# Performance work log

Hardware: AMD Instinct MI355X
Metric: run time of the kernel (lower is better)

The kernel has to match this reference:

```python
import jax, jax.numpy as jnp
import numpy as np

GROUPS = 32
EPS = 1e-5


def setup_inputs() -> dict:
    key = jax.random.key(0)
    ks = jax.random.split(key, 3)
    B, C, H, W, D = 2, 512, 32, 32, 32
    x = jax.random.normal(ks[0], (B, C, H, W, D), dtype=jnp.float32)
    # 1x1 Conv3d weights squeezed to 2-D matrices; fan-in scaled init
    qkv_w = jax.random.normal(ks[1], (3 * C, C), dtype=jnp.float32) / np.sqrt(C)
    qkv_b = jnp.zeros((3 * C,), dtype=jnp.float32)
    proj_w = jax.random.normal(ks[2], (C, C), dtype=jnp.float32) / np.sqrt(C)
    proj_b = jnp.zeros((C,), dtype=jnp.float32)
    gn_w = jnp.ones((C,), dtype=jnp.float32)
    gn_b = jnp.zeros((C,), dtype=jnp.float32)
    return {"x": x, "gn_w": gn_w, "gn_b": gn_b, "qkv_w": qkv_w,
            "qkv_b": qkv_b, "proj_w": proj_w, "proj_b": proj_b}


def _group_norm(x, w, b):
    B, C = x.shape[0], x.shape[1]
    xg = x.reshape(B, GROUPS, C // GROUPS, -1)  # [B, G, C/G, N]
    mean = xg.mean(axis=(2, 3), keepdims=True)
    var = xg.var(axis=(2, 3), keepdims=True)
    xn = ((xg - mean) * jax.lax.rsqrt(var + EPS)).reshape(x.shape)
    shape = (1, C) + (1,) * (x.ndim - 2)
    return xn * w.reshape(shape) + b.reshape(shape)


def reference(x, gn_w, gn_b, qkv_w, qkv_b, proj_w, proj_b):
    B, C, H, W, D = x.shape
    N = H * W * D
    xn = _group_norm(x, gn_w, gn_b)
    xf = xn.reshape(B, C, N)
    # 1x1 conv3d == channel-mixing matmul over flattened spatial tokens
    qkv = jnp.einsum('oc,bcn->bon', qkv_w, xf) + qkv_b[None, :, None]
    q, k, v = jnp.split(qkv, 3, axis=1)  # each [B, C, N]
    scale = 1.0 / (C ** 0.5)
    # NOTE: faithful to source -- attention matrix is [B, C, C] (channel attention)
    attn = jax.nn.softmax(jnp.einsum('bcn,bdn->bcd', q, k) * scale, axis=-1)
    out = jnp.einsum('bcd,bdn->bcn', attn, v)  # [B, C, N]
    proj = jnp.einsum('oc,bcn->bon', proj_w, out) + proj_b[None, :, None]
    return x + proj.reshape(B, C, H, W, D)
```

## Files before the change

### kernel.cpp

```cpp
#include <hip/hip_runtime.h>
#include <cstdint>


typedef unsigned short u16;
typedef unsigned int u32;
typedef __bf16 bf16x8 __attribute__((ext_vector_type(8)));
typedef float f4 __attribute__((ext_vector_type(4)));

#define N_SP 32768
#define C_CH 512
#define NB 2
#define KSPLIT 32
#define LSTR 40

__device__ __forceinline__ float b2f(u16 h){
  union { float f; u32 u; } v; v.u = ((u32)h) << 16; return v.f;
}
__device__ __forceinline__ u16 f2b(float f){
  union { float f; u32 u; } v; v.f = f;
  u32 u = v.u;
  return (u16)((u + 0x7fffu + ((u >> 16) & 1u)) >> 16);
}
__device__ __forceinline__ void split(float v, u16& h, u16& l){
  h = f2b(v);
  l = f2b(v - b2f(h));
}

__global__ void k_zero(float* __restrict__ p, long n){
  long i = (long)blockIdx.x*256 + threadIdx.x;
  if(i < n) p[i] = 0.f;
}

__global__ __launch_bounds__(256) void k_stats(const float* __restrict__ x,
                                               float* __restrict__ cs, float* __restrict__ cq){
  const long bc = blockIdx.x;
  const float* p = x + bc * (long)N_SP;
  const int t = threadIdx.x;
  float s = 0.f, q = 0.f;
  for(int i=0;i<32;i++){
    float4 v = *(const float4*)(p + i*1024 + t*4);
    s += v.x + v.y + v.z + v.w;
    q += v.x*v.x + v.y*v.y + v.z*v.z + v.w*v.w;
  }
  for(int off=32; off; off>>=1){ s += __shfl_down(s, off, 64); q += __shfl_down(q, off, 64); }
  __shared__ float rs[4], rq[4];
  int lane = t & 63, wv = t >> 6;
  if(lane==0){ rs[wv]=s; rq[wv]=q; }
  __syncthreads();
  if(t==0){ cs[bc] = rs[0]+rs[1]+rs[2]+rs[3]; cq[bc] = rq[0]+rq[1]+rq[2]+rq[3]; }
}

__global__ void k_gn(const float* __restrict__ cs, const float* __restrict__ cq,
                     const float* __restrict__ gw, const float* __restrict__ gb,
                     float* __restrict__ s_, float* __restrict__ t_, float* __restrict__ rxn){
  int i = blockIdx.x*blockDim.x + threadIdx.x;
  if(i >= NB*C_CH) return;
  int b = i >> 9, c = i & 511, g = c >> 4;
  int base = (b << 9) | (g << 4);
  float sum=0.f, sq=0.f;
  for(int j=0;j<16;j++){ sum += cs[base+j]; sq += cq[base+j]; }
  const float inv = 1.0f / (16.0f * (float)N_SP);
  float mean = sum * inv;
  float var = sq * inv - mean*mean;
  if(var < 0.f) var = 0.f;
  float rs = rsqrtf(var + 1e-5f);
  float sc = gw[c] * rs;
  float tt = gb[c] - mean * sc;
  s_[i] = sc; t_[i] = tt;
  rxn[i] = sc * cs[i] + (float)N_SP * tt;
}

__global__ __launch_bounds__(256) void k_gram(const float* __restrict__ x, float* __restrict__ Gx){
  __shared__ u16 Ah[128*LSTR], Al[128*LSTR], Bh[128*LSTR], Bl[128*LSTR];
  const int t = threadIdx.x;
  int v = blockIdx.x, ti, tj;
  if(v<4){ti=0;tj=v;} else if(v<7){ti=1;tj=v-3;} else if(v<9){ti=2;tj=v-5;} else {ti=3;tj=3;}
  const int b = blockIdx.z;
  const int i0 = ti << 7, j0 = tj << 7;
  const long xb = (long)b * C_CH * (long)N_SP;
  const int k0 = blockIdx.y * (N_SP / KSPLIT);
  const int lane = t & 63, wave = t >> 6;
  const int wm = wave >> 1, wn = wave & 1;
  const int lr = lane & 15, quad = lane >> 4;
  const int srow = t >> 1, skh = (t & 1) << 4;

  f4 acc[4][4];
  for(int i=0;i<4;i++) for(int j=0;j<4;j++){ f4 z = {0.f,0.f,0.f,0.f}; acc[i][j]=z; }

  const float* gi = x + xb + (long)(i0 + srow)*N_SP + k0 + skh;
  const float* gj = x + xb + (long)(j0 + srow)*N_SP + k0 + skh;

  for(int kk=0; kk<N_SP/KSPLIT; kk+=32){
    float4 va[4], vb[4];
    #pragma unroll
    for(int j2=0;j2<4;j2++){ va[j2] = *(const float4*)(gi + kk + j2*4); vb[j2] = *(const float4*)(gj + kk + j2*4); }
    __syncthreads();
    #pragma unroll
    for(int j2=0;j2<4;j2++){
      float fa[4] = {va[j2].x, va[j2].y, va[j2].z, va[j2].w};
      float fb[4] = {vb[j2].x, vb[j2].y, vb[j2].z, vb[j2].w};
      u16 ha[4], la[4], hb[4], lb[4];
      #pragma unroll
      for(int e=0;e<4;e++){ split(fa[e], ha[e], la[e]); split(fb[e], hb[e], lb[e]); }
      int o = srow*LSTR + skh + j2*4;
      *(uint2*)&Ah[o] = *(uint2*)ha; *(uint2*)&Al[o] = *(uint2*)la;
      *(uint2*)&Bh[o] = *(uint2*)hb; *(uint2*)&Bl[o] = *(uint2*)lb;
    }
    __syncthreads();
    bf16x8 ah[4], al[4], bh[4], bl[4];
    #pragma unroll
    for(int mt=0; mt<4; mt++){
      int o = (wm*64 + mt*16 + lr)*LSTR + quad*8;
      ah[mt] = *(const bf16x8*)&Ah[o]; al[mt] = *(const bf16x8*)&Al[o];
    }
    #pragma unroll
    for(int nt=0; nt<4; nt++){
      int o = (wn*64 + nt*16 + lr)*LSTR + quad*8;
      bh[nt] = *(const bf16x8*)&Bh[o]; bl[nt] = *(const bf16x8*)&Bl[o];
    }
    #pragma unroll
    for(int mt=0; mt<4; mt++)
      #pragma unroll
      for(int nt=0; nt<4; nt++){
        acc[mt][nt] = __builtin_amdgcn_mfma_f32_16x16x32_bf16(ah[mt], bh[nt], acc[mt][nt], 0, 0, 0);
        acc[mt][nt] = __builtin_amdgcn_mfma_f32_16x16x32_bf16(ah[mt], bl[nt], acc[mt][nt], 0, 0, 0);
        acc[mt][nt] = __builtin_amdgcn_mfma_f32_16x16x32_bf16(al[mt], bh[nt], acc[mt][nt], 0, 0, 0);
      }
  }
  const int diff = (ti != tj);
  #pragma unroll
  for(int mt=0; mt<4; mt++){
    #pragma unroll
    for(int nt=0; nt<4; nt++){
      int m = i0 + wm*64 + mt*16 + quad*4;
      int n = j0 + wn*64 + nt*16 + lr;
      #pragma unroll
      for(int r=0;r<4;r++){
        float val = acc[mt][nt][r];
        atomicAdd(Gx + ((long)b*C_CH + m + r)*C_CH + n, val);
        if(diff) atomicAdd(Gx + ((long)b*C_CH + n)*C_CH + m + r, val);
      }
    }
  }
}

__global__ void k_G(const float* __restrict__ Gx, const float* __restrict__ s_,
                    const float* __restrict__ t_, const float* __restrict__ cs,
                    float* __restrict__ G){
  long idx = (long)blockIdx.x*256 + threadIdx.x;
  int j = idx & 511, i = (int)((idx >> 9) & 511), b = (int)(idx >> 18);
  long bo = (long)b << 9;
  float si = s_[bo+i], sj = s_[bo+j], ti = t_[bo+i], tj = t_[bo+j];
  G[idx] = si*sj*Gx[idx] + si*cs[bo+i]*tj + ti*sj*cs[bo+j] + (float)N_SP*ti*tj;
}

__global__ __launch_bounds__(256) void k_mm_nn(const float* __restrict__ A, long sA,
                                               const float* __restrict__ B, long sB,
                                               float* __restrict__ C, long sC){
  __shared__ float As_[16][68];
  __shared__ float Bs_[16][68];
  const int b = blockIdx.z;
  A += (long)b*sA; B += (long)b*sB; C += (long)b*sC;
  const int m0 = (blockIdx.x >> 3) << 6;
  const int n0 = (blockIdx.x & 7) << 6;
  const int t = threadIdx.x;
  const int tm = t >> 4, tn = t & 15;
  float acc[4][4] = {};
  const int ar = t >> 2, ac = (t & 3) << 2;
  const int br = t >> 4, bc = (t & 15) << 2;
  for(int k0=0; k0<512; k0+=16){
    float4 av = *(const float4*)&A[(long)(m0 + ar)*512 + k0 + ac];
    float4 bv = *(const float4*)&B[(long)(k0 + br)*512 + n0 + bc];
    __syncthreads();
    As_[ac+0][ar] = av.x; As_[ac+1][ar] = av.y; As_[ac+2][ar] = av.z; As_[ac+3][ar] = av.w;
    *(float4*)&Bs_[br][bc] = bv;
    __syncthreads();
    #pragma unroll
    for(int k=0;k<16;k++){
      float4 a4 = *(const float4*)&As_[k][tm<<2];
      float4 b4 = *(const float4*)&Bs_[k][tn<<2];
      float aa[4] = {a4.x,a4.y,a4.z,a4.w}, bb[4] = {b4.x,b4.y,b4.z,b4.w};
      #pragma unroll
      for(int i=0;i<4;i++)
        #pragma unroll
        for(int j=0;j<4;j++) acc[i][j] += aa[i]*bb[j];
    }
  }
  for(int i=0;i<4;i++) for(int j=0;j<4;j++)
    C[(long)(m0 + (tm<<2) + i)*512 + n0 + (tn<<2) + j] = acc[i][j];
}

__global__ __launch_bounds__(256) void k_mm_nt_logits(const float* __restrict__ A, long sA,
    const float* __restrict__ Bn, float* __restrict__ C, long sC,
    const float* __restrict__ aq, const float* __restrict__ ak,
    const float* __restrict__ bq, const float* __restrict__ bk, float scale){
  __shared__ float As_[16][68];
  __shared__ float Bs_[16][68];
  const int b = blockIdx.z;
  A += (long)b*sA; C += (long)b*sC;
  const float* aqb = aq + (long)b*512;
  const float* akb = ak + (long)b*512;
  const int m0 = (blockIdx.x >> 3) << 6;
  const int n0 = (blockIdx.x & 7) << 6;
  const int t = threadIdx.x;
  const int tm = t >> 4, tn = t & 15;
  float acc[4][4] = {};
  const int ar = t >> 2, ac = (t & 3) << 2;
  for(int k0=0; k0<512; k0+=16){
    float4 av = *(const float4*)&A[(long)(m0 + ar)*512 + k0 + ac];
    float4 bv = *(const float4*)&Bn[(long)(n0 + ar)*512 + k0 + ac];
    __syncthreads();
    As_[ac+0][ar] = av.x; As_[ac+1][ar] = av.y; As_[ac+2][ar] = av.z; As_[ac+3][ar] = av.w;
    Bs_[ac+0][ar] = bv.x; Bs_[ac+1][ar] = bv.y; Bs_[ac+2][ar] = bv.z; Bs_[ac+3][ar] = bv.w;
    __syncthreads();
    #pragma unroll
    for(int k=0;k<16;k++){
      float4 a4 = *(const float4*)&As_[k][tm<<2];
      float4 b4 = *(const float4*)&Bs_[k][tn<<2];
      float aa[4] = {a4.x,a4.y,a4.z,a4.w}, bb[4] = {b4.x,b4.y,b4.z,b4.w};
      #pragma unroll
      for(int i=0;i<4;i++)
        #pragma unroll
        for(int j=0;j<4;j++) acc[i][j] += aa[i]*bb[j];
    }
  }
  for(int i=0;i<4;i++) for(int j=0;j<4;j++){
    int gi = m0 + (tm<<2) + i, gj = n0 + (tn<<2) + j;
    float vv = acc[i][j] + aqb[gi]*bk[gj] + bq[gi]*(akb[gj] + (float)N_SP*bk[gj]);
    C[(long)gi*512 + gj] = scale*vv;
  }
}

__global__ __launch_bounds__(256) void k_softmax(float* __restrict__ L){
  const long row = blockIdx.x;
  float* p = L + row*512;
  const int t = threadIdx.x;
  float v0 = p[t], v1 = p[t+256];
  float m = fmaxf(v0, v1);
  for(int off=32; off; off>>=1) m = fmaxf(m, __shfl_down(m, off, 64));
  __shared__ float red[4], red2[4];
  int lane = t & 63, wv = t >> 6;
  if(lane==0) red[wv] = m;
  __syncthreads();
  float M = fmaxf(fmaxf(red[0],red[1]), fmaxf(red[2],red[3]));
  float e0 = __expf(v0 - M), e1 = __expf(v1 - M);
  float s = e0 + e1;
  for(int off=32; off; off>>=1) s += __shfl_down(s, off, 64);
  if(lane==0) red2[wv] = s;
  __syncthreads();
  float inv = 1.0f / (red2[0]+red2[1]+red2[2]+red2[3]);
  p[t] = e0*inv; p[t+256] = e1*inv;
}

__global__ __launch_bounds__(128) void k_rowdot(const float* __restrict__ M, long sM,
    const float* __restrict__ v, long sv, float* __restrict__ out, long sout,
    const float* __restrict__ addv, long saddv, int accum){
  const int i = blockIdx.x, b = blockIdx.y;
  const float* Mr = M + (long)b*sM + (long)i*512;
  const float* vb = v + (long)b*sv;
  const int t = threadIdx.x;
  float s = Mr[t]*vb[t] + Mr[t+128]*vb[t+128] + Mr[t+256]*vb[t+256] + Mr[t+384]*vb[t+384];
  for(int off=32; off; off>>=1) s += __shfl_down(s, off, 64);
  __shared__ float r2[2];
  if((t&63)==0) r2[t>>6] = s;
  __syncthreads();
  if(t==0){
    float r = r2[0] + r2[1];
    long oi = (long)b*sout + i;
    if(addv) r += addv[(long)b*saddv + i];
    if(accum) r += out[oi];
    out[oi] = r;
  }
}

__global__ void k_af(const float* __restrict__ A, const float* __restrict__ s_,
                     u16* __restrict__ Afh, u16* __restrict__ Afl){
  long idx = (long)blockIdx.x*256 + threadIdx.x;
  int k = idx & 511; long b = idx >> 18;
  float vv = A[idx] * s_[(b<<9) + k];
  u16 h, l; split(vv, h, l);
  Afh[idx] = h; Afl[idx] = l;
}

__global__ __launch_bounds__(256) void k_final(const u16* __restrict__ Afh, const u16* __restrict__ Afl,
                                               const float* __restrict__ x, const float* __restrict__ cf,
                                               float* __restrict__ y){
  __shared__ u16 Ah[128*LSTR], Al[128*LSTR], Bh[128*LSTR], Bl[128*LSTR];
  const int t = threadIdx.x;
  const int b = blockIdx.z;
  const int n0 = blockIdx.x << 7;
  const int m0 = blockIdx.y << 7;
  const int lane = t & 63, wave = t >> 6;
  const int wm = wave >> 1, wn = wave & 1;
  const int lr = lane & 15, quad = lane >> 4;
  const int arow = t >> 1, akh = (t & 1) << 4;
  const long afb = (long)b*C_CH*C_CH;
  const int kp = (t & 15) << 1;
  const int nq = (t >> 4) << 3;
  const long xb = (long)b*C_CH*(long)N_SP;

  f4 acc[4][4];
  for(int i=0;i<4;i++) for(int j=0;j<4;j++){ f4 z = {0.f,0.f,0.f,0.f}; acc[i][j]=z; }

  for(int kk=0; kk<C_CH; kk+=32){
    const u16* gah = Afh + afb + (long)(m0 + arow)*C_CH + kk + akh;
    const u16* gal = Afl + afb + (long)(m0 + arow)*C_CH + kk + akh;
    uint4 vah0 = *(const uint4*)(gah);
    uint4 vah1 = *(const uint4*)(gah + 8);
    uint4 val0 = *(const uint4*)(gal);
    uint4 val1 = *(const uint4*)(gal + 8);
    const float* gx0 = x + xb + (long)(kk + kp)*N_SP + n0 + nq;
    float4 vx00 = *(const float4*)(gx0);
    float4 vx01 = *(const float4*)(gx0 + 4);
    float4 vx10 = *(const float4*)(gx0 + N_SP);
    float4 vx11 = *(const float4*)(gx0 + N_SP + 4);
    __syncthreads();
    int ao = arow*LSTR + akh;
    *(uint4*)&Ah[ao] = vah0; *(uint4*)&Ah[ao+8] = vah1;
    *(uint4*)&Al[ao] = val0; *(uint4*)&Al[ao+8] = val1;
    float f0[8] = {vx00.x,vx00.y,vx00.z,vx00.w, vx01.x,vx01.y,vx01.z,vx01.w};
    float f1[8] = {vx10.x,vx10.y,vx10.z,vx10.w, vx11.x,vx11.y,vx11.z,vx11.w};
    #pragma unroll
    for(int j=0;j<8;j++){
      u16 h0,l0,h1,l1;
      split(f0[j], h0, l0); split(f1[j], h1, l1);
      int o = (nq + j)*LSTR + kp;
      *(u32*)&Bh[o] = (u32)h0 | ((u32)h1 << 16);
      *(u32*)&Bl[o] = (u32)l0 | ((u32)l1 << 16);
    }
    __syncthreads();
    bf16x8 ah[4], al[4], bh[4], bl[4];
    #pragma unroll
    for(int mt=0; mt<4; mt++){
      int o = (wm*64 + mt*16 + lr)*LSTR + quad*8;
      ah[mt] = *(const bf16x8*)&Ah[o]; al[mt] = *(const bf16x8*)&Al[o];
    }
    #pragma unroll
    for(int nt=0; nt<4; nt++){
      int o = (wn*64 + nt*16 + lr)*LSTR + quad*8;
      bh[nt] = *(const bf16x8*)&Bh[o]; bl[nt] = *(const bf16x8*)&Bl[o];
    }
    #pragma unroll
    for(int mt=0; mt<4; mt++)
      #pragma unroll
      for(int nt=0; nt<4; nt++){
        acc[mt][nt] = __builtin_amdgcn_mfma_f32_16x16x32_bf16(ah[mt], bh[nt], acc[mt][nt], 0, 0, 0);
        acc[mt][nt] = __builtin_amdgcn_mfma_f32_16x16x32_bf16(ah[mt], bl[nt], acc[mt][nt], 0, 0, 0);
        acc[mt][nt] = __builtin_amdgcn_mfma_f32_16x16x32_bf16(al[mt], bh[nt], acc[mt][nt], 0, 0, 0);
      }
  }
  #pragma unroll
  for(int mt=0; mt<4; mt++){
    int mbase = m0 + wm*64 + mt*16 + quad*4;
    float cfv[4];
    #pragma unroll
    for(int r=0;r<4;r++) cfv[r] = cf[b*C_CH + mbase + r];
    #pragma unroll
    for(int nt=0; nt<4; nt++){
      int n = n0 + wn*64 + nt*16 + lr;
      #pragma unroll
      for(int r=0;r<4;r++){
        long idx = xb + (long)(mbase + r)*N_SP + n;
        y[idx] = acc[mt][nt][r] + x[idx] + cfv[r];
      }
    }
  }
}

extern "C" void kernel_launch(void* const* d_in, const int* in_sizes, int n_in,
                              void* d_out, int out_size, void* d_ws, size_t ws_size,
                              hipStream_t stream){
  const float* x    = (const float*)d_in[0];
  const float* gnw  = (const float*)d_in[1];
  const float* gnb  = (const float*)d_in[2];
  const float* qkvw = (const float*)d_in[3];
  const float* qkvb = (const float*)d_in[4];
  const float* pw   = (const float*)d_in[5];
  const float* pb   = (const float*)d_in[6];
  float* y = (float*)d_out;

  char* w = (char*)d_out;
  size_t off = 0;
  auto alloc = [&](size_t bytes)->void*{
    void* p = w + off; off = (off + bytes + 255) & ~(size_t)255; return p;
  };
  float* Gx   = (float*)alloc((size_t)NB*C_CH*C_CH*4);
  float* G    = (float*)alloc((size_t)NB*C_CH*C_CH*4);
  float* T1   = (float*)alloc((size_t)NB*C_CH*C_CH*4);
  float* ATT  = (float*)alloc((size_t)NB*C_CH*C_CH*4);
  float* M0   = (float*)alloc((size_t)NB*C_CH*C_CH*4);
  float* AM   = (float*)alloc((size_t)NB*C_CH*C_CH*4);

  char* w2 = (char*)d_ws;
  size_t off2 = 0;
  auto alloc2 = [&](size_t bytes)->void*{
    void* p = w2 + off2; off2 = (off2 + bytes + 255) & ~(size_t)255; return p;
  };
  u16*   AFH  = (u16*)  alloc2((size_t)NB*C_CH*C_CH*2);
  u16*   AFL  = (u16*)  alloc2((size_t)NB*C_CH*C_CH*2);
  float* CF   = (float*)alloc2(NB*C_CH*4);
  float* CS   = (float*)alloc2(NB*C_CH*4);
  float* CQ   = (float*)alloc2(NB*C_CH*4);
  float* S_   = (float*)alloc2(NB*C_CH*4);
  float* T_   = (float*)alloc2(NB*C_CH*4);
  float* RXN  = (float*)alloc2(NB*C_CH*4);
  float* AQ   = (float*)alloc2(NB*C_CH*4);
  float* AK   = (float*)alloc2(NB*C_CH*4);
  float* E    = (float*)alloc2(NB*C_CH*4);
  (void)ws_size; (void)in_sizes; (void)n_in; (void)out_size;

  const float scale = 0.04419417382415922f;

  k_zero<<<(NB*C_CH*C_CH+255)/256, 256, 0, stream>>>(Gx, (long)NB*C_CH*C_CH);
  k_stats<<<NB*C_CH, 256, 0, stream>>>(x, CS, CQ);
  k_gn<<<4, 256, 0, stream>>>(CS, CQ, gnw, gnb, S_, T_, RXN);
  k_gram<<<dim3(10, KSPLIT, NB), 256, 0, stream>>>(x, Gx);
  k_G<<<(NB*C_CH*C_CH)/256, 256, 0, stream>>>(Gx, S_, T_, CS, G);
  k_mm_nn<<<dim3(64,1,NB), 256, 0, stream>>>(qkvw, 0, G, 262144, T1, 262144);
  k_rowdot<<<dim3(512,NB), 128, 0, stream>>>(qkvw,          0, RXN, 512, AQ, 512, nullptr, 0, 0);
  k_rowdot<<<dim3(512,NB), 128, 0, stream>>>(qkvw+262144,   0, RXN, 512, AK, 512, nullptr, 0, 0);
  k_mm_nt_logits<<<dim3(64,1,NB), 256, 0, stream>>>(T1, 262144, qkvw+262144, ATT, 262144,
                                                    AQ, AK, qkvb, qkvb+512, scale);
  k_softmax<<<NB*C_CH, 256, 0, stream>>>(ATT);
  k_rowdot<<<dim3(512,NB), 128, 0, stream>>>(ATT, 262144, qkvb+1024, 0, E, 512, nullptr, 0, 0);
  k_mm_nn<<<dim3(64,1,NB), 256, 0, stream>>>(ATT, 262144, qkvw+524288, 0, M0, 262144);
  k_mm_nn<<<dim3(64,1,NB), 256, 0, stream>>>(pw, 0, M0, 262144, AM, 262144);
  k_rowdot<<<dim3(512,NB), 128, 0, stream>>>(AM, 262144, T_, 512, CF, 512, nullptr, 0, 0);
  k_rowdot<<<dim3(512,NB), 128, 0, stream>>>(pw, 0, E, 512, CF, 512, pb, 0, 1);
  k_af<<<(NB*C_CH*C_CH)/256, 256, 0, stream>>>(AM, S_, AFH, AFL);
  k_final<<<dim3(N_SP/128, C_CH/128, NB), 256, 0, stream>>>(AFH, AFL, x, CF, y);
}
```

Baseline: 720.7 us.

## Replace gram atomics with split-K partial buffers and a vectorized reduction

The gram kernel now computes all 16 channel tiles per batch instead of only the 10 upper-triangle tiles. Each split-K block writes its tile to a private partial buffer instead of doing atomic adds, and the separate zeroing kernel is removed. The G kernel now sums the 32 partials with float4 loads and applies the group-norm affine correction in the same pass. This trades contended float atomics for about 60% more MFMA work and loads of x in the gram kernel, plus roughly 64 MB of partial-buffer writes and reads.

Measured after the change: 647.6 us. 10.1% less time.

```diff
diff --git a/kernel.cpp b/kernel.cpp
--- a/kernel.cpp
+++ b/kernel.cpp
@@ -24,11 +24,6 @@
 __device__ __forceinline__ void split(float v, u16& h, u16& l){
   h = f2b(v);
   l = f2b(v - b2f(h));
-}
-
-__global__ void k_zero(float* __restrict__ p, long n){
-  long i = (long)blockIdx.x*256 + threadIdx.x;
-  if(i < n) p[i] = 0.f;
 }
 
 __global__ __launch_bounds__(256) void k_stats(const float* __restrict__ x,
@@ -70,11 +65,11 @@
   rxn[i] = sc * cs[i] + (float)N_SP * tt;
 }
 
-__global__ __launch_bounds__(256) void k_gram(const float* __restrict__ x, float* __restrict__ Gx){
+__global__ __launch_bounds__(256) void k_gram(const float* __restrict__ x, float* __restrict__ Gp){
   __shared__ u16 Ah[128*LSTR], Al[128*LSTR], Bh[128*LSTR], Bl[128*LSTR];
   const int t = threadIdx.x;
-  int v = blockIdx.x, ti, tj;
-  if(v<4){ti=0;tj=v;} else if(v<7){ti=1;tj=v-3;} else if(v<9){ti=2;tj=v-5;} else {ti=3;tj=3;}
+  const int tile = blockIdx.x;
+  const int ti = tile >> 2, tj = tile & 3;
   const int b = blockIdx.z;
   const int i0 = ti << 7, j0 = tj << 7;
   const long xb = (long)b * C_CH * (long)N_SP;
@@ -127,31 +122,48 @@
         acc[mt][nt] = __builtin_amdgcn_mfma_f32_16x16x32_bf16(al[mt], bh[nt], acc[mt][nt], 0, 0, 0);
       }
   }
-  const int diff = (ti != tj);
+  float* dst = Gp + ((long)(b*16 + tile)*KSPLIT + blockIdx.y) * 16384;
   #pragma unroll
   for(int mt=0; mt<4; mt++){
     #pragma unroll
     for(int nt=0; nt<4; nt++){
-      int m = i0 + wm*64 + mt*16 + quad*4;
-      int n = j0 + wn*64 + nt*16 + lr;
-      #pragma unroll
-      for(int r=0;r<4;r++){
-        float val = acc[mt][nt][r];
-        atomicAdd(Gx + ((long)b*C_CH + m + r)*C_CH + n, val);
-        if(diff) atomicAdd(Gx + ((long)b*C_CH + n)*C_CH + m + r, val);
-      }
-    }
-  }
-}
-
-__global__ void k_G(const float* __restrict__ Gx, const float* __restrict__ s_,
-                    const float* __restrict__ t_, const float* __restrict__ cs,
-                    float* __restrict__ G){
-  long idx = (long)blockIdx.x*256 + threadIdx.x;
-  int j = idx & 511, i = (int)((idx >> 9) & 511), b = (int)(idx >> 18);
+      int m = wm*64 + mt*16 + quad*4;
+      int n = wn*64 + nt*16 + lr;
+      #pragma unroll
+      for(int r=0;r<4;r++)
+        dst[(m + r)*128 + n] = acc[mt][nt][r];
+    }
+  }
+}
+
+__global__ __launch_bounds__(256) void k_G(const float* __restrict__ Gp, const float* __restrict__ s_,
+                                           const float* __restrict__ t_, const float* __restrict__ cs,
+                                           float* __restrict__ G){
+  long idx4 = ((long)blockIdx.x*256 + threadIdx.x) * 4;
+  int j = (int)(idx4 & 511);
+  int i = (int)((idx4 >> 9) & 511);
+  int b = (int)(idx4 >> 18);
+  int tile = ((i >> 7) << 2) | (j >> 7);
+  int il = i & 127, jl = j & 127;
+  const float* src = Gp + ((long)(b*16 + tile)*KSPLIT) * 16384 + il*128 + jl;
+  float ax=0.f, ay=0.f, az=0.f, aw=0.f;
+  #pragma unroll 4
+  for(int ks=0; ks<KSPLIT; ks++){
+    float4 v = *(const float4*)(src + (long)ks*16384);
+    ax += v.x; ay += v.y; az += v.z; aw += v.w;
+  }
   long bo = (long)b << 9;
-  float si = s_[bo+i], sj = s_[bo+j], ti = t_[bo+i], tj = t_[bo+j];
-  G[idx] = si*sj*Gx[idx] + si*cs[bo+i]*tj + ti*sj*cs[bo+j] + (float)N_SP*ti*tj;
+  float si = s_[bo+i], tii = t_[bo+i], csi = cs[bo+i];
+  float g[4] = {ax, ay, az, aw};
+  float4 out;
+  float* po = (float*)&out;
+  #pragma unroll
+  for(int e=0;e<4;e++){
+    int je = j + e;
+    float sj = s_[bo+je], tj = t_[bo+je], csj = cs[bo+je];
+    po[e] = si*sj*g[e] + si*csi*tj + tii*sj*csj + (float)N_SP*tii*tj;
+  }
+  *(float4*)&G[idx4] = out;
 }
 
 __global__ __launch_bounds__(256) void k_mm_nn(const float* __restrict__ A, long sA,
@@ -384,7 +396,7 @@
   auto alloc = [&](size_t bytes)->void*{
     void* p = w + off; off = (off + bytes + 255) & ~(size_t)255; return p;
   };
-  float* Gx   = (float*)alloc((size_t)NB*C_CH*C_CH*4);
+  float* GP   = (float*)alloc((size_t)NB*16*KSPLIT*16384*4);
   float* G    = (float*)alloc((size_t)NB*C_CH*C_CH*4);
   float* T1   = (float*)alloc((size_t)NB*C_CH*C_CH*4);
   float* ATT  = (float*)alloc((size_t)NB*C_CH*C_CH*4);
@@ -411,11 +423,10 @@
 
   const float scale = 0.04419417382415922f;
 
-  k_zero<<<(NB*C_CH*C_CH+255)/256, 256, 0, stream>>>(Gx, (long)NB*C_CH*C_CH);
   k_stats<<<NB*C_CH, 256, 0, stream>>>(x, CS, CQ);
   k_gn<<<4, 256, 0, stream>>>(CS, CQ, gnw, gnb, S_, T_, RXN);
-  k_gram<<<dim3(10, KSPLIT, NB), 256, 0, stream>>>(x, Gx);
-  k_G<<<(NB*C_CH*C_CH)/256, 256, 0, stream>>>(Gx, S_, T_, CS, G);
+  k_gram<<<dim3(16, KSPLIT, NB), 256, 0, stream>>>(x, GP);
+  k_G<<<512, 256, 0, stream>>>(GP, S_, T_, CS, G);
   k_mm_nn<<<dim3(64,1,NB), 256, 0, stream>>>(qkvw, 0, G, 262144, T1, 262144);
   k_rowdot<<<dim3(512,NB), 128, 0, stream>>>(qkvw,          0, RXN, 512, AQ, 512, nullptr, 0, 0);
   k_rowdot<<<dim3(512,NB), 128, 0, stream>>>(qkvw+262144,   0, RXN, 512, AK, 512, nullptr, 0, 0);
```
